# Kernel optimization log

Measured on AMD Instinct MI355X. Metric: run time of the kernel, lower is better.

Reference implementation:

```python
import jax, jax.numpy as jnp
import numpy as np

B, L, D, NLAYERS, MAX_NODES, DEG = 32, 512, 768, 3, 128, 8


def _build_graph():
    rng = np.random.default_rng(0)
    per = rng.integers(-32, 33, size=B // 2)
    sizes = np.concatenate([96 + per, 96 - per]).astype(np.int64)  # sum = 96*B = 3072, each in [64,128]
    N = int(sizes.sum())
    offs = np.concatenate([[0], np.cumsum(sizes)])
    batch = np.repeat(np.arange(B), sizes).astype(np.int64)
    pad_idx = np.zeros((B, MAX_NODES), np.int64)
    pad_mask = np.zeros((B, MAX_NODES), bool)
    src, dst = [], []
    for b in range(B):
        n = int(sizes[b])
        pad_idx[b, :n] = np.arange(offs[b], offs[b] + n)
        pad_mask[b, :n] = True
        src.append(rng.integers(offs[b], offs[b] + n, n * DEG))
        dst.append(rng.integers(offs[b], offs[b] + n, n * DEG))
    return N, batch, pad_idx, pad_mask, np.concatenate(src), np.concatenate(dst)


def setup_inputs() -> dict:
    N, batch, pad_idx, pad_mask, esrc, edst = _build_graph()
    key = jax.random.key(0)
    ks = jax.random.split(key, 8)
    s = 1.0 / np.sqrt(D)
    return {
        "x": jax.random.normal(ks[0], (N, D), jnp.float32),
        "text": jax.random.normal(ks[1], (B, L, D), jnp.float32),
        "batch_ent1_d_mask": jnp.ones((B, 1), jnp.float32),
        "batch_ent1_g_mask": jnp.ones((B, 1), jnp.float32),
        "gnn_ws": jax.random.normal(ks[2], (NLAYERS, D, D), jnp.float32) * s,
        "gnn_wn": jax.random.normal(ks[3], (NLAYERS, D, D), jnp.float32) * s,
        "gnn_b": jnp.zeros((NLAYERS, D), jnp.float32),
        "atom_w": jax.random.normal(ks[4], (D, D), jnp.float32) * s,
        "atom_b": jnp.zeros((D,), jnp.float32),
        "rand_emb": jax.random.normal(ks[5], (1, D), jnp.float32),
        "batch": jnp.asarray(batch),
        "pad_idx": jnp.asarray(pad_idx),
        "pad_mask": jnp.asarray(pad_mask),
        "edge_src": jnp.asarray(esrc),
        "edge_dst": jnp.asarray(edst),
    }


def reference(x, text, batch_ent1_d_mask, batch_ent1_g_mask, gnn_ws, gnn_wn, gnn_b,
              atom_w, atom_b, rand_emb, batch, pad_idx, pad_mask, edge_src, edge_dst):
    N = x.shape[0]
    E = edge_src.shape[0]
    maskf = pad_mask.astype(x.dtype)            # [B, M]
    n_per = maskf.sum(axis=1)                   # [B] num real nodes per graph
    # edge-neighbor mean counts (constants w.r.t. x)
    cnt = jax.ops.segment_sum(jnp.ones((E,), x.dtype), edge_dst, num_segments=N)
    inv_cnt = 1.0 / jnp.maximum(cnt, 1.0)
    cms = []
    for i in range(NLAYERS):
        # MoleGraphConv stand-in: mean neighbor aggregation + self transform
        msg = jax.ops.segment_sum(x[edge_src], edge_dst, num_segments=N) * inv_cnt[:, None]
        x = jax.nn.relu(x @ gnn_ws[i] + msg @ gnn_wn[i] + gnn_b[i])
        # ragged gather into padded [B, M, D]
        xp = x[pad_idx] * maskf[..., None]
        # graph -> text cross attention (softmax over text tokens; no mask needed)
        g2t = jax.nn.softmax(jnp.einsum('bmd,bld->bml', xp, text), axis=-1)
        g2t_out = jnp.einsum('bml,bld->bmd', g2t, text)            # [B, M, D]
        # text -> graph cross attention (mask padded nodes)
        t2g_logits = jnp.einsum('bld,bmd->blm', text, xp)
        t2g_logits = jnp.where(pad_mask[:, None, :], t2g_logits, jnp.float32(-1e9))
        t2g = jax.nn.softmax(t2g_logits, axis=-1)
        t2g_out = jnp.einsum('blm,bmd->bld', t2g, xp)              # [B, L, D]
        # mean over concatenated rows [n_i + L] per graph (pool_type=2)
        pooled = ((g2t_out * maskf[..., None]).sum(axis=1) + t2g_out.sum(axis=1)) \
                 / (n_per + jnp.float32(L))[:, None]
        cms.append(pooled)
    out_cms = jnp.mean(jnp.stack(cms, axis=1), axis=1)              # mean over layers
    out_t = text[:, 0, :]
    # scatter-mean of final node features per graph
    gsum = jax.ops.segment_sum(x, batch, num_segments=B)
    gcnt = jax.ops.segment_sum(jnp.ones((N,), x.dtype), batch, num_segments=B)
    xg = gsum / jnp.maximum(gcnt, 1.0)[:, None]
    # dropout is a no-op in eval mode
    out_g = jnp.tanh(xg @ atom_w + atom_b)
    z = rand_emb[0]
    dg = batch_ent1_d_mask * batch_ent1_g_mask
    return jnp.concatenate([
        out_t * batch_ent1_d_mask + (1 - batch_ent1_d_mask) * z,
        out_g * batch_ent1_g_mask + (1 - batch_ent1_g_mask) * z,
        out_cms * dg + (1 - dg) * z,
    ], axis=-1)
```

## Files before the change

### kernel.cpp

```cpp
#include <hip/hip_runtime.h>

#define D 768
#define B 32
#define L 512
#define M 128
#define NNODES 3072
#define NEDGES 24576

using bf16x8 = __attribute__((ext_vector_type(8))) short;
using f32x4  = __attribute__((ext_vector_type(4))) float;

__device__ __forceinline__ float bf2f(unsigned short u) {
  union { unsigned int i; float f; } v; v.i = ((unsigned int)u) << 16; return v.f;
}
__device__ __forceinline__ unsigned short f2bf(float f) {
  union { float f; unsigned int i; } v; v.f = f;
  unsigned int x = v.i;
  return (unsigned short)((x + 0x7FFFu + ((x >> 16) & 1u)) >> 16);
}
__device__ __forceinline__ float ldf(const void* p, size_t i, int f32) {
  return f32 ? ((const float*)p)[i] : bf2f(((const unsigned short*)p)[i]);
}
__device__ __forceinline__ int ldi(const void* p, size_t i, int w64) {
  return w64 ? (int)((const long long*)p)[i] : ((const int*)p)[i];
}
__device__ __forceinline__ f32x4 mfma16(bf16x8 a, bf16x8 b, f32x4 c) {
  return __builtin_amdgcn_mfma_f32_16x16x32_bf16(a, b, c, 0, 0, 0);
}
__device__ __forceinline__ void gl_lds(const unsigned short* gsrc, unsigned short* lbase,
                                       int lane) {
  __builtin_amdgcn_global_load_lds(
      (const __attribute__((address_space(1))) unsigned int*)(gsrc + lane * 8),
      (__attribute__((address_space(3))) unsigned int*)lbase, 16, 0, 0);
}

__device__ __forceinline__ float pk_read(const unsigned short* P, int p, int l, int d) {
  return bf2f(P[(((size_t)(p * 24 + (d >> 5))) << 9) + ((((d & 31) >> 3) << 4) + l) * 8 + (d & 7)]);
}


__device__ void d_pack_in(const void* src, unsigned short* rows, unsigned short* dst,
                          int p, int tid, int f, char* smem) {
  unsigned short* buf = (unsigned short*)smem;
#pragma unroll
  for (int j = 0; j < 6; ++j) {
    int idx = j * 256 + tid;
    int r = idx / 96, c = idx % 96;
    size_t sbase = (size_t)(p * 16 + r) * 768 + c * 8;
    union { unsigned short v[8]; uint4 q; } u;
    if (f) {
      const float* sp = (const float*)src + sbase;
#pragma unroll
      for (int e = 0; e < 8; ++e) u.v[e] = f2bf(sp[e]);
    } else {
      const unsigned short* sp = (const unsigned short*)src + sbase;
#pragma unroll
      for (int e = 0; e < 8; ++e) u.v[e] = sp[e];
    }
    if (rows) *(uint4*)&rows[sbase] = u.q;
    int lpos = (c >> 2) * 64 + (c & 3) * 16 + r;
#pragma unroll
    for (int e = 0; e < 8; ++e) buf[lpos * 8 + e] = u.v[e];
  }
  __syncthreads();
  uint4* d4 = (uint4*)(dst + (size_t)p * 12288);
  const uint4* b4 = (const uint4*)buf;
#pragma unroll
  for (int j = 0; j < 6; ++j) d4[j * 256 + tid] = b4[j * 256 + tid];
}

__device__ void d_pack(const unsigned short* src, unsigned short* dst,
                       int p, int tid, char* smem) {
  unsigned short* buf = (unsigned short*)smem;
#pragma unroll
  for (int j = 0; j < 6; ++j) {
    int idx = j * 256 + tid;
    int r = idx / 96, c = idx % 96;
    size_t sbase = (size_t)(p * 16 + r) * 768 + c * 8;
    uint4 q = *(const uint4*)(src + sbase);
    int lpos = (c >> 2) * 64 + (c & 3) * 16 + r;
    *(uint4*)&buf[lpos * 8] = q;
  }
  __syncthreads();
  uint4* d4 = (uint4*)(dst + (size_t)p * 12288);
  const uint4* b4 = (const uint4*)buf;
#pragma unroll
  for (int j = 0; j < 6; ++j) d4[j * 256 + tid] = b4[j * 256 + tid];
}

__device__ void d_wpack(const void* Ws, const void* Wn, const void* Aw, int f,
                        unsigned short* WsPk, unsigned short* WnPk, unsigned short* AwPk,
                        int r0, int tid, char* smem) {
  unsigned short* buf = (unsigned short*)smem;
  int z = r0 / 288, rem = r0 % 288;
  int nblk = rem % 12, kk = rem / 12;
  const void* src; unsigned short* dst; size_t zoff;
  if (z < 3)      { src = Ws; zoff = (size_t)z * D * D;       dst = WsPk + zoff; }
  else if (z < 6) { src = Wn; zoff = (size_t)(z - 3) * D * D; dst = WnPk + zoff; }
  else            { src = Aw; zoff = 0;                       dst = AwPk; }
  int n0 = nblk * 64;
  int kl = tid >> 3, c8 = tid & 7;
  size_t sbase = zoff + (size_t)(kk * 32 + kl) * D + n0 + c8 * 8;
  unsigned short v[8];
  if (f) {
    const float* sp = (const float*)src + sbase;
#pragma unroll
    for (int e = 0; e < 8; ++e) v[e] = f2bf(sp[e]);
  } else {
    const unsigned short* sp = (const unsigned short*)src + sbase;
#pragma unroll
    for (int e = 0; e < 8; ++e) v[e] = sp[e];
  }
  int ebit = kl & 7, quad = kl >> 3;
#pragma unroll
  for (int i = 0; i < 8; ++i) {
    int nl = c8 * 8 + i;
    int pl = nl >> 4;
    int lane = quad * 16 + (nl & 15);
    buf[pl * 512 + lane * 8 + ebit] = v[i];
  }
  __syncthreads();
  int pl = tid >> 6, pos = tid & 63;
  int pG = nblk * 4 + pl;
  uint4 q = *(const uint4*)&buf[pl * 512 + pos * 8];
  *(uint4*)&dst[(((size_t)(pG * 24 + kk)) << 9) + pos * 8] = q;
}

__device__ void d_count(const void* edst, const void* batch, int w,
                        int* cnt, int* gcnt, int i) {
  if (i < NEDGES) atomicAdd(&cnt[ldi(edst, i, w)], 1);
  if (i < NNODES) atomicAdd(&gcnt[ldi(batch, i, w)], 1);
}

__device__ void d_msg(const unsigned short* x, const int* cnt, const int* rowstart,
                      const int* csr, unsigned short* Mpk, int p, int tid, char* smem) {
  unsigned short* buf = (unsigned short*)smem;
  int w = tid >> 6, lane = tid & 63;
#pragma unroll
  for (int i = 0; i < 4; ++i) {
    int r = w * 4 + i;
    int n = p * 16 + r;
    int deg = cnt[n], base = rowstart[n];
    float inv = 1.0f / (float)(deg > 1 ? deg : 1);
    float a[12];
#pragma unroll
    for (int j = 0; j < 12; ++j) a[j] = 0.f;
    for (int e = 0; e < deg; ++e) {
      const uint2* xr = (const uint2*)(x + (size_t)csr[base + e] * D);
#pragma unroll
      for (int j = 0; j < 3; ++j) {
        uint2 v = xr[lane + j * 64];
        a[j * 4 + 0] += bf2f((unsigned short)(v.x & 0xFFFFu));
        a[j * 4 + 1] += bf2f((unsigned short)(v.x >> 16));
        a[j * 4 + 2] += bf2f((unsigned short)(v.y & 0xFFFFu));
        a[j * 4 + 3] += bf2f((unsigned short)(v.y >> 16));
      }
    }
#pragma unroll
    for (int j = 0; j < 3; ++j) {
      int d0 = (lane + j * 64) * 4;
      int c = d0 >> 3, e0 = d0 & 7;
      int lpos = (c >> 2) * 64 + (c & 3) * 16 + r;
      unsigned short* bp = &buf[lpos * 8 + e0];
      bp[0] = f2bf(a[j * 4 + 0] * inv);
      bp[1] = f2bf(a[j * 4 + 1] * inv);
      bp[2] = f2bf(a[j * 4 + 2] * inv);
      bp[3] = f2bf(a[j * 4 + 3] * inv);
    }
  }
  __syncthreads();
  uint4* d4 = (uint4*)(Mpk + (size_t)p * 12288);
  const uint4* b4 = (const uint4*)buf;
#pragma unroll
  for (int j = 0; j < 6; ++j) d4[j * 256 + tid] = b4[j * 256 + tid];
}

__device__ void d_gemm(const unsigned short* Xpk, const unsigned short* Mpk,
                       const unsigned short* WsPk, const unsigned short* WnPk,
                       const void* bias, size_t bias_off, int f,
                       unsigned short* Y, int bx, int by, int tid, char* smem) {
  unsigned short* lds = (unsigned short*)smem;
  int wave = tid >> 6, lane = tid & 63;
  int q = lane >> 4, t = lane & 15;
  int wm = wave >> 1, wn = wave & 1;
  int pa = bx * 4, pb = by * 4;
  f32x4 acc[2][2];
#pragma unroll
  for (int mi = 0; mi < 2; ++mi)
#pragma unroll
    for (int ni = 0; ni < 2; ++ni)
      acc[mi][ni] = (f32x4){0.f, 0.f, 0.f, 0.f};
  int c0 = wave * 2;
  int pan0 = (wave < 2) ? (pa + c0) : (pb + c0 - 4);
  for (int r = 0; r < 8; ++r) {
    int h = r >> 2;
    int kk0 = r * 6 - h * 24;
    const unsigned short* P = (wave < 2) ? (h ? Mpk : Xpk) : (h ? WnPk : WsPk);
#pragma unroll
    for (int st = 0; st < 6; ++st) {
      gl_lds(P + (((size_t)(pan0 * 24 + kk0 + st)) << 9), &lds[st * 4096 + c0 * 512], lane);
      gl_lds(P + (((size_t)((pan0 + 1) * 24 + kk0 + st)) << 9), &lds[st * 4096 + (c0 + 1) * 512], lane);
    }
    __syncthreads();
#pragma unroll
    for (int st = 0; st < 6; ++st) {
      bf16x8 a0 = *(const bf16x8*)&lds[st * 4096 + (wm * 2 + 0) * 512 + lane * 8];
      bf16x8 a1 = *(const bf16x8*)&lds[st * 4096 + (wm * 2 + 1) * 512 + lane * 8];
      bf16x8 b0 = *(const bf16x8*)&lds[st * 4096 + (4 + wn * 2 + 0) * 512 + lane * 8];
      bf16x8 b1 = *(const bf16x8*)&lds[st * 4096 + (4 + wn * 2 + 1) * 512 + lane * 8];
      acc[0][0] = mfma16(a0, b0, acc[0][0]);
      acc[0][1] = mfma16(a0, b1, acc[0][1]);
      acc[1][0] = mfma16(a1, b0, acc[1][0]);
      acc[1][1] = mfma16(a1, b1, acc[1][1]);
    }
    __syncthreads();
  }
#pragma unroll
  for (int ni = 0; ni < 2; ++ni) {
    int col = by * 64 + wn * 32 + ni * 16 + t;
    float bv = ldf(bias, bias_off + col, f);
#pragma unroll
    for (int mi = 0; mi < 2; ++mi) {
#pragma unroll
      for (int r = 0; r < 4; ++r) {
        int row = bx * 64 + wm * 32 + mi * 16 + q * 4 + r;
        float v = acc[mi][ni][r] + bv;
        Y[(size_t)row * D + col] = f2bf(v > 0.f ? v : 0.f);
      }
    }
  }
}

__device__ void d_xp(const unsigned short* Xn, const void* pidx, int w64,
                     const int* gcnt, unsigned short* xp, unsigned short* XpPk,
                     float* xgacc, int p, int tid, char* smem) {
  unsigned short* rows = (unsigned short*)smem;
  int r = tid >> 4, c16 = tid & 15;
  int bm = p * 16 + r;
  int b = bm >> 7, m = bm & 127;
  int nb = gcnt[b];
  uint4* dl = (uint4*)&rows[r * 776];
  if (m < nb) {
    const uint4* srcr = (const uint4*)(Xn + (size_t)ldi(pidx, bm, w64) * D);
#pragma unroll
    for (int j = 0; j < 6; ++j) dl[c16 + j * 16] = srcr[c16 + j * 16];
  } else {
    uint4 z = {0u, 0u, 0u, 0u};
#pragma unroll
    for (int j = 0; j < 6; ++j) dl[c16 + j * 16] = z;
  }
  __syncthreads();
#pragma unroll
  for (int j = 0; j < 6; ++j) {
    int idx = j * 256 + tid;
    int rr = idx / 96, cc = idx % 96;
    uint4 vv = *(const uint4*)&rows[rr * 776 + cc * 8];
    *(uint4*)&xp[(size_t)(p * 16 + rr) * D + cc * 8] = vv;
  }
  unsigned short* pb = XpPk + (size_t)p * 12288;
#pragma unroll
  for (int j = 0; j < 6; ++j) {
    int odx = j * 256 + tid;
    int kk = odx >> 6, lanep = odx & 63;
    int rr = lanep & 15, cg = lanep >> 4;
    int cc = kk * 4 + cg;
    uint4 vv = *(const uint4*)&rows[rr * 776 + cc * 8];
    *(uint4*)&pb[odx * 8] = vv;
  }
  if (xgacc) {
    int bb = p >> 3;
#pragma unroll
    for (int j = 0; j < 3; ++j) {
      int d = j * 256 + tid;
      float s = 0.f;
#pragma unroll
      for (int rr = 0; rr < 16; ++rr) s += bf2f(rows[rr * 776 + d]);
      atomicAdd(&xgacc[(size_t)bb * D + d], s);
    }
  }
}

__device__ void d_scores(const unsigned short* XpPk, const unsigned short* Tpk,
                         float* S, int bx, int by, int bz, int tid, char* smem) {
  unsigned short* lds = (unsigned short*)smem;
  int wave = tid >> 6, lane = tid & 63;
  int q = lane >> 4, t = lane & 15;
  int wm = wave >> 1, wn = wave & 1;
  int pa = bz * 8 + bx * 4;
  int pb = bz * 32 + by * 4;
  f32x4 acc[2][2];
#pragma unroll
  for (int mi = 0; mi < 2; ++mi)
#pragma unroll
    for (int ni = 0; ni < 2; ++ni)
      acc[mi][ni] = (f32x4){0.f, 0.f, 0.f, 0.f};
  int c0 = wave * 2;
  const unsigned short* P = (wave < 2) ? XpPk : Tpk;
  int pan0 = (wave < 2) ? (pa + c0) : (pb + c0 - 4);
  for (int r = 0; r < 4; ++r) {
    int kk0 = r * 6;
#pragma unroll
    for (int st = 0; st < 6; ++st) {
      gl_lds(P + (((size_t)(pan0 * 24 + kk0 + st)) << 9), &lds[st * 4096 + c0 * 512], lane);
      gl_lds(P + (((size_t)((pan0 + 1) * 24 + kk0 + st)) << 9), &lds[st * 4096 + (c0 + 1) * 512], lane);
    }
    __syncthreads();
#pragma unroll
    for (int st = 0; st < 6; ++st) {
      bf16x8 a0 = *(const bf16x8*)&lds[st * 4096 + (wm * 2 + 0) * 512 + lane * 8];
      bf16x8 a1 = *(const bf16x8*)&lds[st * 4096 + (wm * 2 + 1) * 512 + lane * 8];
      bf16x8 b0 = *(const bf16x8*)&lds[st * 4096 + (4 + wn * 2 + 0) * 512 + lane * 8];
      bf16x8 b1 = *(const bf16x8*)&lds[st * 4096 + (4 + wn * 2 + 1) * 512 + lane * 8];
      acc[0][0] = mfma16(a0, b0, acc[0][0]);
      acc[0][1] = mfma16(a0, b1, acc[0][1]);
      acc[1][0] = mfma16(a1, b0, acc[1][0]);
      acc[1][1] = mfma16(a1, b1, acc[1][1]);
    }
    __syncthreads();
  }
  float* Sb = S + (size_t)bz * M * L;
#pragma unroll
  for (int ni = 0; ni < 2; ++ni) {
    int col = by * 64 + wn * 32 + ni * 16 + t;
#pragma unroll
    for (int mi = 0; mi < 2; ++mi) {
#pragma unroll
      for (int r = 0; r < 4; ++r) {
        int row = bx * 64 + wm * 32 + mi * 16 + q * 4 + r;
        Sb[(size_t)row * L + col] = acc[mi][ni][r];
      }
    }
  }
}

__device__ void d_stats(const float* S, const int* gcnt, float* rmax, float* rsum,
                        float* cmaxv, float* csumv, int bid, int tid, char* smem) {
  if (bid < B * M) {
    float* red = (float*)smem;
    int lane = tid & 63, wv = tid >> 6;
    const float* r = S + (size_t)bid * L;
    float s0 = r[tid], s1 = r[tid + 256];
    float m = fmaxf(s0, s1);
#pragma unroll
    for (int o = 32; o > 0; o >>= 1) m = fmaxf(m, __shfl_down(m, o));
    if (lane == 0) red[wv] = m;
    __syncthreads();
    float bm = fmaxf(fmaxf(red[0], red[1]), fmaxf(red[2], red[3]));
    __syncthreads();
    float e = __expf(s0 - bm) + __expf(s1 - bm);
#pragma unroll
    for (int o = 32; o > 0; o >>= 1) e += __shfl_down(e, o);
    if (lane == 0) red[wv] = e;
    __syncthreads();
    if (tid == 0) { rmax[bid] = bm; rsum[bid] = red[0] + red[1] + red[2] + red[3]; }
  } else {
    float (*pm)[64] = (float(*)[64])smem;
    float (*ps)[64] = (float(*)[64])(smem + 1024);
    int cid = bid - B * M;
    int b = cid >> 3, ly = cid & 7;
    int w = tid >> 6, lane = tid & 63;
    int l = ly * 64 + lane;
    int nb = gcnt[b];
    const float* Sb = S + (size_t)b * M * L;
    int m0 = w * 32, m1 = min(m0 + 32, nb);
    float cm = -1e30f, cs = 0.f;
    for (int m = m0; m < m1; ++m) {
      float s = Sb[(size_t)m * L + l];
      if (s > cm) { cs = cs * __expf(cm - s) + 1.f; cm = s; }
      else cs += __expf(s - cm);
    }
    pm[w][lane] = cm; ps[w][lane] = cs;
    __syncthreads();
    if (w == 0) {
      float CM = -1e30f;
#pragma unroll
      for (int j = 0; j < 4; ++j) CM = fmaxf(CM, pm[j][lane]);
      float CS = 0.f;
#pragma unroll
      for (int j = 0; j < 4; ++j) CS += ps[j][lane] * __expf(pm[j][lane] - CM);
      cmaxv[b * L + l] = CM; csumv[b * L + l] = CS;
    }
  }
}

__device__ void d_cross(const float* S, const float* rmax, const float* rsum,
                        const float* cmaxv, const float* csumv, const int* gcnt,
                        float* wv, float* t2gcol, int bid, int tid, char* smem) {
  if (bid < 256) {
    float* rm = (float*)smem;
    float* ri = (float*)(smem + 512);
    float (*pw)[64] = (float(*)[64])(smem + 1024);
    int b = bid >> 3, ly = bid & 7;
    int w = tid >> 6, lane = tid & 63;
    if (tid < M) { rm[tid] = rmax[b * M + tid]; ri[tid] = 1.f / rsum[b * M + tid]; }
    __syncthreads();
    int l = ly * 64 + lane;
    int nb = gcnt[b];
    const float* Sb = S + (size_t)b * M * L;
    int m0 = w * 32, m1 = min(m0 + 32, nb);
    float wp = 0.f;
    for (int m = m0; m < m1; ++m)
      wp += __expf(Sb[(size_t)m * L + l] - rm[m]) * ri[m];
    pw[w][lane] = wp;
    __syncthreads();
    if (w == 0)
      wv[b * L + l] = pw[0][lane] + pw[1][lane] + pw[2][lane] + pw[3][lane];
  } else {
    float* red = (float*)smem;
    int bm = bid - 256;
    int b = bm >> 7, m = bm & 127;
    int lane = tid & 63, w = tid >> 6;
    int nb = gcnt[b];
    float acc = 0.f;
    if (m < nb) {
      const float* r = S + (size_t)bm * L;
      const float* cm = cmaxv + b * L;
      const float* cs = csumv + b * L;
      acc = __expf(r[tid] - cm[tid]) / cs[tid]
          + __expf(r[tid + 256] - cm[tid + 256]) / cs[tid + 256];
    }
#pragma unroll
    for (int o = 32; o > 0; o >>= 1) acc += __shfl_down(acc, o);
    if (lane == 0) red[w] = acc;
    __syncthreads();
    if (tid == 0) t2gcol[bm] = red[0] + red[1] + red[2] + red[3];
  }
}

__device__ void d_pooled(const float* wv, const float* t2gcol, const unsigned short* Tpk,
                         const unsigned short* xp, const int* gcnt, float* pooled,
                         int bid, int tid) {
  int b = bid & 31;
  int rest = bid >> 5;
  int y = rest % 3, c = rest / 3;
  int d = y * 256 + tid;
  float acc = 0.f;
  if (c < 8) {
    int l0 = c * 64;
    for (int l = l0; l < l0 + 64; ++l) {
      int p = b * 32 + (l >> 4);
      acc += wv[b * L + l] * pk_read(Tpk, p, l & 15, d);
    }
  } else {
    const unsigned short* Xb = xp + (size_t)b * M * D;
    int mm0 = (c - 8) * 64;
    for (int m = mm0; m < mm0 + 64; ++m) acc += t2gcol[b * M + m] * bf2f(Xb[(size_t)m * D + d]);
  }
  atomicAdd(&pooled[(size_t)b * D + d], acc / ((float)gcnt[b] + 512.f));
}

__device__ void d_atom(const float* xgacc, const int* gcnt, const unsigned short* AwPk,
                       float* gpre, int bid, int tid) {
  int w = tid >> 6, lane = tid & 63;
  int q = lane >> 4, t = lane & 15;
  int nbase = bid * 64 + w * 16;
  int pb = nbase >> 4;
  int n0 = gcnt[t], n1 = gcnt[16 + t];
  float inv0 = 1.f / (float)(n0 > 1 ? n0 : 1);
  float inv1 = 1.f / (float)(n1 > 1 ? n1 : 1);
  f32x4 acc[2];
  acc[0] = (f32x4){0.f, 0.f, 0.f, 0.f};
  acc[1] = (f32x4){0.f, 0.f, 0.f, 0.f};
  for (int kk = 0; kk < 24; ++kk) {
    const float* s0 = xgacc + (size_t)t * D + kk * 32 + q * 8;
    const float* s1 = xgacc + (size_t)(16 + t) * D + kk * 32 + q * 8;
    union { unsigned short v[8]; bf16x8 f; } a0, a1;
#pragma unroll
    for (int j = 0; j < 8; ++j) { a0.v[j] = f2bf(s0[j] * inv0); a1.v[j] = f2bf(s1[j] * inv1); }
    bf16x8 bv = *(const bf16x8*)(AwPk + (((size_t)(pb * 24 + kk)) << 9) + (lane << 3));
    acc[0] = mfma16(a0.f, bv, acc[0]);
    acc[1] = mfma16(a1.f, bv, acc[1]);
  }
#pragma unroll
  for (int mi = 0; mi < 2; ++mi)
#pragma unroll
    for (int r = 0; r < 4; ++r) {
      int row = mi * 16 + q * 4 + r;
      gpre[(size_t)row * D + nbase + t] = acc[mi][r];
    }
}


__global__ void k_init(int* cnt, int* cursor, int* gcnt, float* pooled, float* xgacc,
                       const unsigned short* __restrict__ t,
                       const unsigned int* __restrict__ e, int* __restrict__ flags) {
  int i = blockIdx.x * 256 + threadIdx.x;
  if (i < NNODES) { cnt[i] = 0; cursor[i] = 0; }
  if (i < B) gcnt[i] = 0;
  if (i < B * D) { pooled[i] = 0.f; xgacc[i] = 0.f; }
  if (blockIdx.x == 0) {
    __shared__ int r0[256];
    __shared__ unsigned r1[256];
    int tid = threadIdx.x;
    int bad = 0;
    for (int j = tid; j < 8192; j += 256) {
      unsigned short u = t[2 * j];
      unsigned ex = (u >> 7) & 0xFF;
      if (ex >= 0xC0) bad = 1;
    }
    unsigned o = 0;
    for (int j = tid; j < NEDGES / 2; j += 256) o |= e[2 * j + 1];
    r0[tid] = bad; r1[tid] = o;
    __syncthreads();
    for (int s = 128; s > 0; s >>= 1) {
      if (tid < s) { r0[tid] |= r0[tid + s]; r1[tid] |= r1[tid + s]; }
      __syncthreads();
    }
    if (tid == 0) { flags[0] = r0[0]; flags[1] = (r1[0] == 0) ? 1 : 0; }
  }
}

__global__ __launch_bounds__(256) void k_setup2(
    const void* x_in, unsigned short* x0, unsigned short* PkA,
    const void* text, unsigned short* Tpk,
    const void* Ws, const void* Wn, const void* Aw,
    unsigned short* WsPk, unsigned short* WnPk, unsigned short* AwPk,
    const void* edst, const void* batch, int* cnt, int* gcnt,
    const int* __restrict__ flags) {
  extern __shared__ char smem[];
  int bid = blockIdx.x, tid = threadIdx.x;
  if (bid < 1216) {
    int f = flags[0];
    if (bid < NNODES / 16) d_pack_in(x_in, x0, PkA, bid, tid, f, smem);
    else d_pack_in(text, nullptr, Tpk, bid - NNODES / 16, tid, f, smem);
  } else if (bid < 3232) {
    d_wpack(Ws, Wn, Aw, flags[0], WsPk, WnPk, AwPk, bid - 1216, tid, smem);
  } else {
    d_count(edst, batch, flags[1], cnt, gcnt, (bid - 3232) * 256 + tid);
  }
}

__global__ void k_scan(const int* __restrict__ cnt, int* __restrict__ rowstart) {
  __shared__ int a[NNODES], b[NNODES];
  int tid = threadIdx.x;
  for (int i = tid; i < NNODES; i += 1024) a[i] = cnt[i];
  __syncthreads();
  int* s = a; int* d = b;
  for (int off = 1; off < NNODES; off <<= 1) {
    for (int i = tid; i < NNODES; i += 1024)
      d[i] = s[i] + (i >= off ? s[i - off] : 0);
    __syncthreads();
    int* t = s; s = d; d = t;
  }
  for (int i = tid; i < NNODES; i += 1024) rowstart[i + 1] = s[i];
  if (tid == 0) rowstart[0] = 0;
}

__global__ void k_scatter(const void* __restrict__ esrc, const void* __restrict__ edst,
                          const int* __restrict__ flags, const int* __restrict__ rowstart,
                          int* __restrict__ cursor, int* __restrict__ csr) {
  int w = flags[1];
  int i = blockIdx.x * 256 + threadIdx.x;
  if (i < NEDGES) {
    int dd = ldi(edst, i, w);
    int pos = atomicAdd(&cursor[dd], 1);
    csr[rowstart[dd] + pos] = ldi(esrc, i, w);
  }
}

__global__ __launch_bounds__(256) void k_msgp(
    const unsigned short* x, const int* cnt, const int* rowstart, const int* csr,
    unsigned short* Mpk) {
  extern __shared__ char smem[];
  d_msg(x, cnt, rowstart, csr, Mpk, blockIdx.x, threadIdx.x, smem);
}

__global__ __launch_bounds__(256) void k_gemm(
    const unsigned short* Apk, const unsigned short* Mpk,
    const unsigned short* WsPk, const unsigned short* WnPk,
    const void* bias, unsigned long bias_off, const int* flags, unsigned short* Y) {
  extern __shared__ char smem[];
  int g = blockIdx.x;
  d_gemm(Apk, Mpk, WsPk, WnPk, bias, bias_off, flags[0], Y, g % 48, g / 48,
         threadIdx.x, smem);
}

__global__ __launch_bounds__(256) void k_postg(
    const unsigned short* Y, unsigned short* Npk, int packN,
    const void* pidx, const int* flags, const int* gcnt,
    unsigned short* xp, unsigned short* XpPk, float* xgacc) {
  extern __shared__ char smem[];
  int bid = blockIdx.x, tid = threadIdx.x;
  if (bid < packN) d_pack(Y, Npk, bid, tid, smem);
  else d_xp(Y, pidx, flags[1], gcnt, xp, XpPk, xgacc, bid - packN, tid, smem);
}

__global__ __launch_bounds__(256) void k_scmsg(
    const unsigned short* XpPk, const unsigned short* Tpk, float* S,
    int msgN, const unsigned short* x, const int* cnt, const int* rowstart,
    const int* csr, unsigned short* Mpk) {
  extern __shared__ char smem[];
  int bid = blockIdx.x, tid = threadIdx.x;
  if (bid < 512) d_scores(XpPk, Tpk, S, bid & 1, (bid >> 1) & 7, bid >> 4, tid, smem);
  else d_msg(x, cnt, rowstart, csr, Mpk, bid - 512, tid, smem);
}

__global__ __launch_bounds__(256) void k_stgemm(
    const float* S, const int* gcnt, float* rmax, float* rsum, float* cmaxv, float* csumv,
    int gemmN, const unsigned short* Apk, const unsigned short* Mpk,
    const unsigned short* WsPk, const unsigned short* WnPk,
    const void* bias, unsigned long bias_off, const int* flags, unsigned short* Y) {
  extern __shared__ char smem[];
  int bid = blockIdx.x, tid = threadIdx.x;
  if (bid < 4352) d_stats(S, gcnt, rmax, rsum, cmaxv, csumv, bid, tid, smem);
  else {
    int g = bid - 4352;
    d_gemm(Apk, Mpk, WsPk, WnPk, bias, bias_off, flags[0], Y, g % 48, g / 48, tid, smem);
  }
}

__global__ __launch_bounds__(256) void k_crpostg(
    const float* S, const float* rmax, const float* rsum, const float* cmaxv,
    const float* csumv, const int* gcnt, float* wv, float* t2gcol,
    int packN, int xpN, const unsigned short* Y, unsigned short* Npk,
    const void* pidx, const int* flags, unsigned short* xp, unsigned short* XpPk,
    float* xgacc) {
  extern __shared__ char smem[];
  int bid = blockIdx.x, tid = threadIdx.x;
  if (bid < 4352) d_cross(S, rmax, rsum, cmaxv, csumv, gcnt, wv, t2gcol, bid, tid, smem);
  else {
    int r = bid - 4352;
    if (r < packN) d_pack(Y, Npk, r, tid, smem);
    else d_xp(Y, pidx, flags[1], gcnt, xp, XpPk, xgacc, r - packN, tid, smem);
  }
}

__global__ __launch_bounds__(256) void k_plscmsg(
    const float* wv, const float* t2gcol, const unsigned short* Tpk,
    const unsigned short* xpL, const int* gcnt, float* pooled,
    int scN, const unsigned short* XpPk, float* S,
    int msgN, const unsigned short* x, const int* cnt, const int* rowstart,
    const int* csr, unsigned short* Mpk,
    int atomN, const float* xgacc, const unsigned short* AwPk, float* gpre) {
  extern __shared__ char smem[];
  int bid = blockIdx.x, tid = threadIdx.x;
  if (bid < 960) { d_pooled(wv, t2gcol, Tpk, xpL, gcnt, pooled, bid, tid); return; }
  int r = bid - 960;
  if (r < scN) { d_scores(XpPk, Tpk, S, r & 1, (r >> 1) & 7, r >> 4, tid, smem); return; }
  r -= scN;
  if (r < msgN) { d_msg(x, cnt, rowstart, csr, Mpk, r, tid, smem); return; }
  d_atom(xgacc, gcnt, AwPk, gpre, r - msgN, tid);
}

__global__ __launch_bounds__(256) void k_final(
    const unsigned short* __restrict__ Tpk, const float* __restrict__ gpre,
    const float* __restrict__ pooled, const void* __restrict__ ab,
    const void* __restrict__ dmask, const void* __restrict__ gmask,
    const void* __restrict__ remb, const int* __restrict__ flags,
    void* __restrict__ out) {
  int f = flags[0];
  int b = blockIdx.x, tid = threadIdx.x;
  float dm = ldf(dmask, b, f);
  float gm = ldf(gmask, b, f);
  float dg = dm * gm;
  size_t base = (size_t)b * 2304;
#pragma unroll
  for (int j = 0; j < 3; ++j) {
    int d = tid + j * 256;
    float z = ldf(remb, d, f);
    float tv = pk_read(Tpk, b * 32, 0, d);
    float o0 = tv * dm + (1.f - dm) * z;
    float gv = tanhf(gpre[(size_t)b * D + d] + ldf(ab, d, f));
    float o1 = gv * gm + (1.f - gm) * z;
    float p = pooled[(size_t)b * D + d] * (1.f / 3.f);
    float o2 = p * dg + (1.f - dg) * z;
    if (f) {
      float* of = (float*)out;
      of[base + d] = o0; of[base + 768 + d] = o1; of[base + 1536 + d] = o2;
    } else {
      unsigned short* ob = (unsigned short*)out;
      ob[base + d] = f2bf(o0); ob[base + 768 + d] = f2bf(o1); ob[base + 1536 + d] = f2bf(o2);
    }
  }
}

extern "C" void kernel_launch(void* const* d_in, const int* in_sizes, int n_in,
                              void* d_out, int out_size, void* d_ws, size_t ws_size,
                              hipStream_t stream) {
  const void* x_in  = d_in[0];
  const void* text  = d_in[1];
  const void* dmask = d_in[2];
  const void* gmask = d_in[3];
  const void* gws   = d_in[4];
  const void* gwn   = d_in[5];
  const void* gb    = d_in[6];
  const void* aw    = d_in[7];
  const void* ab    = d_in[8];
  const void* remb  = d_in[9];
  const void* batch = d_in[10];
  const void* pidx  = d_in[11];
  const void* esrc  = d_in[13];
  const void* edst  = d_in[14];

  char* wsp = (char*)d_ws;
  size_t off = 0;
  auto carve = [&](size_t bytes) -> void* {
    void* p = wsp + off;
    off += (bytes + 255) & ~(size_t)255;
    return p;
  };
  int* flags = (int*)carve(2 * 4);
  unsigned short* x0    = (unsigned short*)carve((size_t)NNODES * D * 2);
  unsigned short* xA    = (unsigned short*)carve((size_t)NNODES * D * 2);
  unsigned short* xB    = (unsigned short*)carve((size_t)NNODES * D * 2);
  unsigned short* PkA   = (unsigned short*)carve((size_t)NNODES * D * 2);
  unsigned short* PkB   = (unsigned short*)carve((size_t)NNODES * D * 2);
  unsigned short* Mpk   = (unsigned short*)carve((size_t)NNODES * D * 2);
  unsigned short* Tpk   = (unsigned short*)carve((size_t)B * L * D * 2);
  unsigned short* WsPk  = (unsigned short*)carve((size_t)3 * D * D * 2);
  unsigned short* WnPk  = (unsigned short*)carve((size_t)3 * D * D * 2);
  unsigned short* AwPk  = (unsigned short*)carve((size_t)D * D * 2);
  unsigned short* xpA   = (unsigned short*)carve((size_t)B * M * D * 2);
  unsigned short* xpB   = (unsigned short*)carve((size_t)B * M * D * 2);
  unsigned short* XpPkA = (unsigned short*)carve((size_t)B * M * D * 2);
  unsigned short* XpPkB = (unsigned short*)carve((size_t)B * M * D * 2);
  float* xgacc   = (float*)carve((size_t)B * D * 4);
  float* gpre    = (float*)carve((size_t)B * D * 4);
  float* S       = (float*)carve((size_t)B * M * L * 4);
  float* rmax    = (float*)carve((size_t)B * M * 4);
  float* rsum    = (float*)carve((size_t)B * M * 4);
  float* wv      = (float*)carve((size_t)B * L * 4);
  float* cmaxv   = (float*)carve((size_t)B * L * 4);
  float* csumv   = (float*)carve((size_t)B * L * 4);
  float* t2gcol  = (float*)carve((size_t)B * M * 4);
  float* pooled  = (float*)carve((size_t)B * D * 4);
  int* cnt      = (int*)carve((size_t)NNODES * 4);
  int* rowstart = (int*)carve((size_t)(NNODES + 1) * 4);
  int* cursor   = (int*)carve((size_t)NNODES * 4);
  int* gcnt     = (int*)carve((size_t)B * 4);
  int* csr      = (int*)carve((size_t)NEDGES * 4);

  const size_t DD = (size_t)D * D;

  k_init<<<96, 256, 0, stream>>>(cnt, cursor, gcnt, pooled, xgacc,
                                 (const unsigned short*)text, (const unsigned int*)edst, flags);
  k_setup2<<<3328, 256, 24576, stream>>>(x_in, x0, PkA, text, Tpk, gws, gwn, aw,
                                         WsPk, WnPk, AwPk, edst, batch, cnt, gcnt, flags);
  k_scan<<<1, 1024, 0, stream>>>(cnt, rowstart);
  k_scatter<<<96, 256, 0, stream>>>(esrc, edst, flags, rowstart, cursor, csr);

  k_msgp<<<192, 256, 24576, stream>>>(x0, cnt, rowstart, csr, Mpk);
  k_gemm<<<576, 256, 49152, stream>>>(PkA, Mpk, WsPk, WnPk, gb, 0, flags, xA);
  k_postg<<<448, 256, 24832, stream>>>(xA, PkB, 192, pidx, flags, gcnt, xpA, XpPkA, nullptr);
  k_scmsg<<<704, 256, 49152, stream>>>(XpPkA, Tpk, S, 192, xA, cnt, rowstart, csr, Mpk);
  k_stgemm<<<4928, 256, 49152, stream>>>(S, gcnt, rmax, rsum, cmaxv, csumv,
                                         576, PkB, Mpk, WsPk + DD, WnPk + DD, gb, D, flags, xB);
  k_crpostg<<<4800, 256, 24832, stream>>>(S, rmax, rsum, cmaxv, csumv, gcnt, wv, t2gcol,
                                          192, 256, xB, PkA, pidx, flags, xpB, XpPkB, nullptr);
  k_plscmsg<<<1664, 256, 49152, stream>>>(wv, t2gcol, Tpk, xpA, gcnt, pooled,
                                          512, XpPkB, S, 192, xB, cnt, rowstart, csr, Mpk,
                                          0, nullptr, nullptr, nullptr);
  k_stgemm<<<4928, 256, 49152, stream>>>(S, gcnt, rmax, rsum, cmaxv, csumv,
                                         576, PkA, Mpk, WsPk + 2 * DD, WnPk + 2 * DD,
                                         gb, 2 * D, flags, xA);
  k_crpostg<<<4608, 256, 24832, stream>>>(S, rmax, rsum, cmaxv, csumv, gcnt, wv, t2gcol,
                                          0, 256, xA, nullptr, pidx, flags, xpA, XpPkA, xgacc);
  k_plscmsg<<<1472, 256, 49152, stream>>>(wv, t2gcol, Tpk, xpB, gcnt, pooled,
                                          512, XpPkA, S, 0, nullptr, nullptr, nullptr,
                                          nullptr, nullptr, 0, nullptr, nullptr, nullptr);
  k_stgemm<<<4352, 256, 2048, stream>>>(S, gcnt, rmax, rsum, cmaxv, csumv,
                                        0, nullptr, nullptr, nullptr, nullptr,
                                        nullptr, 0, flags, nullptr);
  k_crpostg<<<4352, 256, 2048, stream>>>(S, rmax, rsum, cmaxv, csumv, gcnt, wv, t2gcol,
                                         0, 0, nullptr, nullptr, pidx, flags,
                                         nullptr, nullptr, nullptr);
  k_plscmsg<<<972, 256, 2048, stream>>>(wv, t2gcol, Tpk, xpA, gcnt, pooled,
                                        0, nullptr, nullptr, 0, nullptr, nullptr, nullptr,
                                        nullptr, nullptr, 12, xgacc, AwPk, gpre);
  k_final<<<32, 256, 0, stream>>>(Tpk, gpre, pooled, ab, dmask, gmask, remb, flags, d_out);
}
```

Before: 455.9 us.

## Double-buffer GEMM/score K-loop and vectorize pooled reduction with fewer blocks

The GEMM and score tiles now stream one K-step at a time into a two-slot LDS ring, issuing the next async load before computing the current one. This replaces the old pattern of loading six steps and then computing, and it cuts LDS per block from 48KB to 16KB, which allows more blocks to be resident per CU. The pooled reduction now uses 16-byte vector loads with 8 accumulators per thread over 10 segments per graph, so it needs 320 blocks instead of 960 and issues fewer atomics. In exchange there is one barrier per K-step with only one step of prefetch, which may leave load latency exposed.

```diff
diff --git a/kernel.cpp b/kernel.cpp
--- a/kernel.cpp
+++ b/kernel.cpp
@@ -36,6 +36,15 @@
 
 __device__ __forceinline__ float pk_read(const unsigned short* P, int p, int l, int d) {
   return bf2f(P[(((size_t)(p * 24 + (d >> 5))) << 9) + ((((d & 31) >> 3) << 4) + l) * 8 + (d & 7)]);
+}
+
+__device__ __forceinline__ void fma8(float* acc, float w, uint4 v) {
+  unsigned xs[4] = {v.x, v.y, v.z, v.w};
+#pragma unroll
+  for (int j = 0; j < 4; ++j) {
+    acc[2 * j]     += w * bf2f((unsigned short)(xs[j] & 0xFFFFu));
+    acc[2 * j + 1] += w * bf2f((unsigned short)(xs[j] >> 16));
+  }
 }
 
 
@@ -192,27 +201,27 @@
       acc[mi][ni] = (f32x4){0.f, 0.f, 0.f, 0.f};
   int c0 = wave * 2;
   int pan0 = (wave < 2) ? (pa + c0) : (pb + c0 - 4);
-  for (int r = 0; r < 8; ++r) {
-    int h = r >> 2;
-    int kk0 = r * 6 - h * 24;
+  auto issue = [&](int s) {
+    int h = (s >= 24);
     const unsigned short* P = (wave < 2) ? (h ? Mpk : Xpk) : (h ? WnPk : WsPk);
-#pragma unroll
-    for (int st = 0; st < 6; ++st) {
-      gl_lds(P + (((size_t)(pan0 * 24 + kk0 + st)) << 9), &lds[st * 4096 + c0 * 512], lane);
-      gl_lds(P + (((size_t)((pan0 + 1) * 24 + kk0 + st)) << 9), &lds[st * 4096 + (c0 + 1) * 512], lane);
-    }
-    __syncthreads();
-#pragma unroll
-    for (int st = 0; st < 6; ++st) {
-      bf16x8 a0 = *(const bf16x8*)&lds[st * 4096 + (wm * 2 + 0) * 512 + lane * 8];
-      bf16x8 a1 = *(const bf16x8*)&lds[st * 4096 + (wm * 2 + 1) * 512 + lane * 8];
-      bf16x8 b0 = *(const bf16x8*)&lds[st * 4096 + (4 + wn * 2 + 0) * 512 + lane * 8];
-      bf16x8 b1 = *(const bf16x8*)&lds[st * 4096 + (4 + wn * 2 + 1) * 512 + lane * 8];
-      acc[0][0] = mfma16(a0, b0, acc[0][0]);
-      acc[0][1] = mfma16(a0, b1, acc[0][1]);
-      acc[1][0] = mfma16(a1, b0, acc[1][0]);
-      acc[1][1] = mfma16(a1, b1, acc[1][1]);
-    }
+    int kk = h ? (s - 24) : s;
+    unsigned short* dst = &lds[(s & 1) * 4096 + c0 * 512];
+    gl_lds(P + (((size_t)(pan0 * 24 + kk)) << 9), dst, lane);
+    gl_lds(P + (((size_t)((pan0 + 1) * 24 + kk)) << 9), dst + 512, lane);
+  };
+  issue(0);
+  __syncthreads();
+  for (int s = 0; s < 48; ++s) {
+    if (s < 47) issue(s + 1);
+    const unsigned short* bs = &lds[(s & 1) * 4096];
+    bf16x8 a0 = *(const bf16x8*)&bs[(wm * 2 + 0) * 512 + lane * 8];
+    bf16x8 a1 = *(const bf16x8*)&bs[(wm * 2 + 1) * 512 + lane * 8];
+    bf16x8 b0 = *(const bf16x8*)&bs[(4 + wn * 2 + 0) * 512 + lane * 8];
+    bf16x8 b1 = *(const bf16x8*)&bs[(4 + wn * 2 + 1) * 512 + lane * 8];
+    acc[0][0] = mfma16(a0, b0, acc[0][0]);
+    acc[0][1] = mfma16(a0, b1, acc[0][1]);
+    acc[1][0] = mfma16(a1, b0, acc[1][0]);
+    acc[1][1] = mfma16(a1, b1, acc[1][1]);
     __syncthreads();
   }
 #pragma unroll
@@ -297,25 +306,24 @@
   int c0 = wave * 2;
   const unsigned short* P = (wave < 2) ? XpPk : Tpk;
   int pan0 = (wave < 2) ? (pa + c0) : (pb + c0 - 4);
-  for (int r = 0; r < 4; ++r) {
-    int kk0 = r * 6;
-#pragma unroll
-    for (int st = 0; st < 6; ++st) {
-      gl_lds(P + (((size_t)(pan0 * 24 + kk0 + st)) << 9), &lds[st * 4096 + c0 * 512], lane);
-      gl_lds(P + (((size_t)((pan0 + 1) * 24 + kk0 + st)) << 9), &lds[st * 4096 + (c0 + 1) * 512], lane);
-    }
-    __syncthreads();
-#pragma unroll
-    for (int st = 0; st < 6; ++st) {
-      bf16x8 a0 = *(const bf16x8*)&lds[st * 4096 + (wm * 2 + 0) * 512 + lane * 8];
-      bf16x8 a1 = *(const bf16x8*)&lds[st * 4096 + (wm * 2 + 1) * 512 + lane * 8];
-      bf16x8 b0 = *(const bf16x8*)&lds[st * 4096 + (4 + wn * 2 + 0) * 512 + lane * 8];
-      bf16x8 b1 = *(const bf16x8*)&lds[st * 4096 + (4 + wn * 2 + 1) * 512 + lane * 8];
-      acc[0][0] = mfma16(a0, b0, acc[0][0]);
-      acc[0][1] = mfma16(a0, b1, acc[0][1]);
-      acc[1][0] = mfma16(a1, b0, acc[1][0]);
-      acc[1][1] = mfma16(a1, b1, acc[1][1]);
-    }
+  auto issue = [&](int s) {
+    unsigned short* dst = &lds[(s & 1) * 4096 + c0 * 512];
+    gl_lds(P + (((size_t)(pan0 * 24 + s)) << 9), dst, lane);
+    gl_lds(P + (((size_t)((pan0 + 1) * 24 + s)) << 9), dst + 512, lane);
+  };
+  issue(0);
+  __syncthreads();
+  for (int s = 0; s < 24; ++s) {
+    if (s < 23) issue(s + 1);
+    const unsigned short* bs = &lds[(s & 1) * 4096];
+    bf16x8 a0 = *(const bf16x8*)&bs[(wm * 2 + 0) * 512 + lane * 8];
+    bf16x8 a1 = *(const bf16x8*)&bs[(wm * 2 + 1) * 512 + lane * 8];
+    bf16x8 b0 = *(const bf16x8*)&bs[(4 + wn * 2 + 0) * 512 + lane * 8];
+    bf16x8 b1 = *(const bf16x8*)&bs[(4 + wn * 2 + 1) * 512 + lane * 8];
+    acc[0][0] = mfma16(a0, b0, acc[0][0]);
+    acc[0][1] = mfma16(a0, b1, acc[0][1]);
+    acc[1][0] = mfma16(a1, b0, acc[1][0]);
+    acc[1][1] = mfma16(a1, b1, acc[1][1]);
     __syncthreads();
   }
   float* Sb = S + (size_t)bz * M * L;
@@ -429,24 +437,52 @@
 
 __device__ void d_pooled(const float* wv, const float* t2gcol, const unsigned short* Tpk,
                          const unsigned short* xp, const int* gcnt, float* pooled,
-                         int bid, int tid) {
-  int b = bid & 31;
-  int rest = bid >> 5;
-  int y = rest % 3, c = rest / 3;
-  int d = y * 256 + tid;
-  float acc = 0.f;
-  if (c < 8) {
-    int l0 = c * 64;
-    for (int l = l0; l < l0 + 64; ++l) {
-      int p = b * 32 + (l >> 4);
-      acc += wv[b * L + l] * pk_read(Tpk, p, l & 15, d);
-    }
-  } else {
-    const unsigned short* Xb = xp + (size_t)b * M * D;
-    int mm0 = (c - 8) * 64;
-    for (int m = mm0; m < mm0 + 64; ++m) acc += t2gcol[b * M + m] * bf2f(Xb[(size_t)m * D + d]);
-  }
-  atomicAdd(&pooled[(size_t)b * D + d], acc / ((float)gcnt[b] + 512.f));
+                         int bid, int tid, char* smem) {
+  float* lred = (float*)smem;
+  float* wbuf = (float*)(smem + 3072);
+  int b = bid / 10, seg = bid - b * 10;
+  int chunk = tid % 96, half = tid / 96;
+  int d = chunk * 8;
+  float acc[8];
+#pragma unroll
+  for (int j = 0; j < 8; ++j) acc[j] = 0.f;
+  if (tid < 64) {
+    wbuf[tid] = (seg < 8) ? wv[b * L + seg * 64 + tid]
+                          : t2gcol[b * M + (seg - 8) * 64 + tid];
+  }
+  __syncthreads();
+  if (half < 2) {
+    if (seg < 8) {
+      int pbase = b * 32 + seg * 4;
+      size_t cbase = ((size_t)(d >> 5)) << 9;
+      int coff = ((d & 31) >> 3) << 4;
+      for (int i = 0; i < 32; ++i) {
+        int l = half * 32 + i;
+        const unsigned short* src =
+            Tpk + (((size_t)((pbase + (l >> 4)) * 24)) << 9) + cbase +
+            (size_t)(coff + (l & 15)) * 8;
+        fma8(acc, wbuf[l], *(const uint4*)src);
+      }
+    } else {
+      const unsigned short* Xb = xp + (size_t)b * M * D + d;
+      int m0 = (seg - 8) * 64;
+      for (int i = 0; i < 32; ++i) {
+        int mm = half * 32 + i;
+        fma8(acc, wbuf[mm], *(const uint4*)&Xb[(size_t)(m0 + mm) * D]);
+      }
+    }
+  }
+  if (half == 1) {
+#pragma unroll
+    for (int j = 0; j < 8; ++j) lred[chunk * 8 + j] = acc[j];
+  }
+  __syncthreads();
+  if (half == 0) {
+    float inv = 1.f / ((float)gcnt[b] + 512.f);
+#pragma unroll
+    for (int j = 0; j < 8; ++j)
+      atomicAdd(&pooled[(size_t)b * D + d + j], (acc[j] + lred[chunk * 8 + j]) * inv);
+  }
 }
 
 __device__ void d_atom(const float* xgacc, const int* gcnt, const unsigned short* AwPk,
@@ -634,8 +670,8 @@
     int atomN, const float* xgacc, const unsigned short* AwPk, float* gpre) {
   extern __shared__ char smem[];
   int bid = blockIdx.x, tid = threadIdx.x;
-  if (bid < 960) { d_pooled(wv, t2gcol, Tpk, xpL, gcnt, pooled, bid, tid); return; }
-  int r = bid - 960;
+  if (bid < 320) { d_pooled(wv, t2gcol, Tpk, xpL, gcnt, pooled, bid, tid, smem); return; }
+  int r = bid - 320;
   if (r < scN) { d_scores(XpPk, Tpk, S, r & 1, (r >> 1) & 7, r >> 4, tid, smem); return; }
   r -= scN;
   if (r < msgN) { d_msg(x, cnt, rowstart, csr, Mpk, r, tid, smem); return; }
@@ -740,31 +776,31 @@
   k_scatter<<<96, 256, 0, stream>>>(esrc, edst, flags, rowstart, cursor, csr);
 
   k_msgp<<<192, 256, 24576, stream>>>(x0, cnt, rowstart, csr, Mpk);
-  k_gemm<<<576, 256, 49152, stream>>>(PkA, Mpk, WsPk, WnPk, gb, 0, flags, xA);
+  k_gemm<<<576, 256, 16384, stream>>>(PkA, Mpk, WsPk, WnPk, gb, 0, flags, xA);
   k_postg<<<448, 256, 24832, stream>>>(xA, PkB, 192, pidx, flags, gcnt, xpA, XpPkA, nullptr);
-  k_scmsg<<<704, 256, 49152, stream>>>(XpPkA, Tpk, S, 192, xA, cnt, rowstart, csr, Mpk);
-  k_stgemm<<<4928, 256, 49152, stream>>>(S, gcnt, rmax, rsum, cmaxv, csumv,
+  k_scmsg<<<704, 256, 24576, stream>>>(XpPkA, Tpk, S, 192, xA, cnt, rowstart, csr, Mpk);
+  k_stgemm<<<4928, 256, 16384, stream>>>(S, gcnt, rmax, rsum, cmaxv, csumv,
                                          576, PkB, Mpk, WsPk + DD, WnPk + DD, gb, D, flags, xB);
   k_crpostg<<<4800, 256, 24832, stream>>>(S, rmax, rsum, cmaxv, csumv, gcnt, wv, t2gcol,
                                           192, 256, xB, PkA, pidx, flags, xpB, XpPkB, nullptr);
-  k_plscmsg<<<1664, 256, 49152, stream>>>(wv, t2gcol, Tpk, xpA, gcnt, pooled,
+  k_plscmsg<<<1024, 256, 24576, stream>>>(wv, t2gcol, Tpk, xpA, gcnt, pooled,
                                           512, XpPkB, S, 192, xB, cnt, rowstart, csr, Mpk,
                                           0, nullptr, nullptr, nullptr);
-  k_stgemm<<<4928, 256, 49152, stream>>>(S, gcnt, rmax, rsum, cmaxv, csumv,
+  k_stgemm<<<4928, 256, 16384, stream>>>(S, gcnt, rmax, rsum, cmaxv, csumv,
                                          576, PkA, Mpk, WsPk + 2 * DD, WnPk + 2 * DD,
                                          gb, 2 * D, flags, xA);
   k_crpostg<<<4608, 256, 24832, stream>>>(S, rmax, rsum, cmaxv, csumv, gcnt, wv, t2gcol,
                                           0, 256, xA, nullptr, pidx, flags, xpA, XpPkA, xgacc);
-  k_plscmsg<<<1472, 256, 49152, stream>>>(wv, t2gcol, Tpk, xpB, gcnt, pooled,
-                                          512, XpPkA, S, 0, nullptr, nullptr, nullptr,
-                                          nullptr, nullptr, 0, nullptr, nullptr, nullptr);
+  k_plscmsg<<<832, 256, 24576, stream>>>(wv, t2gcol, Tpk, xpB, gcnt, pooled,
+                                         512, XpPkA, S, 0, nullptr, nullptr, nullptr,
+                                         nullptr, nullptr, 0, nullptr, nullptr, nullptr);
   k_stgemm<<<4352, 256, 2048, stream>>>(S, gcnt, rmax, rsum, cmaxv, csumv,
                                         0, nullptr, nullptr, nullptr, nullptr,
                                         nullptr, 0, flags, nullptr);
   k_crpostg<<<4352, 256, 2048, stream>>>(S, rmax, rsum, cmaxv, csumv, gcnt, wv, t2gcol,
                                          0, 0, nullptr, nullptr, pidx, flags,
                                          nullptr, nullptr, nullptr);
-  k_plscmsg<<<972, 256, 2048, stream>>>(wv, t2gcol, Tpk, xpA, gcnt, pooled,
+  k_plscmsg<<<332, 256, 4096, stream>>>(wv, t2gcol, Tpk, xpA, gcnt, pooled,
                                         0, nullptr, nullptr, 0, nullptr, nullptr, nullptr,
                                         nullptr, nullptr, 12, xgacc, AwPk, gpre);
   k_final<<<32, 256, 0, stream>>>(Tpk, gpre, pooled, ab, dmask, gmask, remb, flags, d_out);
```

New measurement: 649.1 us. 42.4% more time.
